# Kernel tuning notes

Measured on AMD Instinct MI355X. Metric: run time of the kernel, lower is better.

Reference implementation:

```python
import jax, jax.numpy as jnp
import numpy as np

EPS = 1e-5


def _bn(a, gamma, beta):
    # training-mode BatchNorm1d applied independently at each timestep:
    # statistics over the batch axis (axis=1) of a [T, B, H] tensor (biased var).
    mu = a.mean(axis=1, keepdims=True)
    var = a.var(axis=1, keepdims=True)
    return gamma * (a - mu) * jax.lax.rsqrt(var + EPS) + beta


def _layer(x, W_xz, b_xz, g_z, beta_z, W_hz, b_hz, W_xh, b_xh, g_h, beta_h, W_hh, b_hh):
    # Precompute the input-side projections + BN for all timesteps (one big GEMM),
    # then scan only the recurrent part.
    az = _bn(jnp.einsum('tbi,hi->tbh', x, W_xz) + b_xz, g_z, beta_z)  # [T,B,H]
    ah = _bn(jnp.einsum('tbi,hi->tbh', x, W_xh) + b_xh, g_h, beta_h)  # [T,B,H]
    B = x.shape[1]
    H = W_hz.shape[0]

    def step(h, inp):
        az_t, ah_t = inp
        Z = jax.nn.sigmoid(az_t + h @ W_hz.T + b_hz)
        Ht = jax.nn.relu(ah_t + h @ W_hh.T + b_hh)
        h2 = Z * h + (1.0 - Z) * Ht
        return h2, h2

    h0 = jnp.zeros((B, H), x.dtype)
    _, ys = jax.lax.scan(step, h0, (az, ah))
    return ys  # [T,B,H]


def setup_inputs() -> dict:
    key = jax.random.key(0)
    T, B, I, H = 500, 64, 512, 1024
    ks = iter(jax.random.split(key, 24))

    def rn(shape, fan):
        return jax.random.normal(next(ks), shape, jnp.float32) / np.sqrt(fan)

    d = {"x": jax.random.normal(next(ks), (T, B, I), jnp.float32)}
    for l, fin in enumerate([I, H]):
        d[f"W_xz{l}"] = rn((H, fin), fin)
        d[f"b_xz{l}"] = rn((H,), fin)
        d[f"g_z{l}"] = jnp.ones((H,), jnp.float32)
        d[f"beta_z{l}"] = jnp.zeros((H,), jnp.float32)
        d[f"W_hz{l}"] = rn((H, H), H)
        d[f"b_hz{l}"] = rn((H,), H)
        d[f"W_xh{l}"] = rn((H, fin), fin)
        d[f"b_xh{l}"] = rn((H,), fin)
        d[f"g_h{l}"] = jnp.ones((H,), jnp.float32)
        d[f"beta_h{l}"] = jnp.zeros((H,), jnp.float32)
        d[f"W_hh{l}"] = rn((H, H), H)
        d[f"b_hh{l}"] = rn((H,), H)
    return d


def reference(x,
              W_xz0, b_xz0, g_z0, beta_z0, W_hz0, b_hz0, W_xh0, b_xh0, g_h0, beta_h0, W_hh0, b_hh0,
              W_xz1, b_xz1, g_z1, beta_z1, W_hz1, b_hz1, W_xh1, b_xh1, g_h1, beta_h1, W_hh1, b_hh1):
    h = _layer(x, W_xz0, b_xz0, g_z0, beta_z0, W_hz0, b_hz0,
               W_xh0, b_xh0, g_h0, beta_h0, W_hh0, b_hh0)
    h = _layer(h, W_xz1, b_xz1, g_z1, beta_z1, W_hz1, b_hz1,
               W_xh1, b_xh1, g_h1, beta_h1, W_hh1, b_hh1)
    return h  # [T, B, hidden_size]
```

## Files before the change

### kernel.cpp

```cpp
#include <hip/hip_runtime.h>

#define TT 500
#define NB_BATCH 64
#define HID 1024
#define NC 2048

typedef __attribute__((ext_vector_type(8))) __bf16 bf16x8;
typedef __attribute__((ext_vector_type(8))) unsigned short us8;
typedef __attribute__((ext_vector_type(4))) unsigned short us4;
typedef __attribute__((ext_vector_type(4))) float f32x4;
typedef __attribute__((ext_vector_type(2))) unsigned long long u64x2;

__device__ __forceinline__ unsigned short f2bf(float f) {
  unsigned u = __builtin_bit_cast(unsigned, f);
  u += 0x7fffu + ((u >> 16) & 1u);
  return (unsigned short)(u >> 16);
}
__device__ __forceinline__ float bf2f(unsigned short h) {
  unsigned u = ((unsigned)h) << 16;
  return __builtin_bit_cast(float, u);
}
__device__ __forceinline__ bf16x8 ld_bf8(const unsigned short* p) {
  return __builtin_bit_cast(bf16x8, *(const us8*)p);
}

#define XS_STR 40
#define WS_STR 40

__global__ __launch_bounds__(256) void proj_bn_kernel(
    const float* __restrict__ X, int K,
    const float* __restrict__ Wxz, const float* __restrict__ Wxh,
    const float* __restrict__ gz, const float* __restrict__ bz,
    const float* __restrict__ gh, const float* __restrict__ bh,
    unsigned short* __restrict__ A)
{
  __shared__ unsigned short Xs[64 * XS_STR];
  __shared__ unsigned short Ws[128 * WS_STR];

  const int t   = blockIdx.x >> 4;
  const int nt  = blockIdx.x & 15;
  const int tid = threadIdx.x;
  const int wave = tid >> 6;
  const int lane = tid & 63;
  const int lm = lane & 15;
  const int lq = lane >> 4;

  const float* Wsrc = (nt < 8) ? (Wxz + (size_t)(nt * 128) * K)
                               : (Wxh + (size_t)((nt - 8) * 128) * K);
  const float* Xbase = X + (size_t)(t * 64) * K;

  f32x4 acc[4][2];
#pragma unroll
  for (int i = 0; i < 4; i++)
#pragma unroll
    for (int j = 0; j < 2; j++) acc[i][j] = (f32x4){0.f, 0.f, 0.f, 0.f};

  const int nkt = K >> 5;
  for (int kt = 0; kt < nkt; ++kt) {
    const int k0 = kt << 5;
#pragma unroll
    for (int it = 0; it < 2; ++it) {
      int idx = it * 256 + tid;
      int r = idx >> 3, c4 = idx & 7;
      float4 v = *(const float4*)(Xbase + (size_t)r * K + k0 + c4 * 4);
      us4 o; o[0] = f2bf(v.x); o[1] = f2bf(v.y); o[2] = f2bf(v.z); o[3] = f2bf(v.w);
      *(us4*)&Xs[r * XS_STR + c4 * 4] = o;
    }
#pragma unroll
    for (int it = 0; it < 4; ++it) {
      int idx = it * 256 + tid;
      int r = idx >> 3, c4 = idx & 7;
      float4 v = *(const float4*)(Wsrc + (size_t)r * K + k0 + c4 * 4);
      us4 o; o[0] = f2bf(v.x); o[1] = f2bf(v.y); o[2] = f2bf(v.z); o[3] = f2bf(v.w);
      *(us4*)&Ws[r * WS_STR + c4 * 4] = o;
    }
    __syncthreads();
    bf16x8 bfr0 = ld_bf8(&Ws[(wave * 32 + lm) * WS_STR + lq * 8]);
    bf16x8 bfr1 = ld_bf8(&Ws[(wave * 32 + 16 + lm) * WS_STR + lq * 8]);
#pragma unroll
    for (int rt = 0; rt < 4; ++rt) {
      bf16x8 afr = ld_bf8(&Xs[(rt * 16 + lm) * XS_STR + lq * 8]);
      acc[rt][0] = __builtin_amdgcn_mfma_f32_16x16x32_bf16(afr, bfr0, acc[rt][0], 0, 0, 0);
      acc[rt][1] = __builtin_amdgcn_mfma_f32_16x16x32_bf16(afr, bfr1, acc[rt][1], 0, 0, 0);
    }
    __syncthreads();
  }

  const float inv64 = 1.0f / 64.0f;
#pragma unroll
  for (int ct = 0; ct < 2; ++ct) {
    float s1 = 0.f, s2 = 0.f;
#pragma unroll
    for (int rt = 0; rt < 4; ++rt)
#pragma unroll
      for (int r = 0; r < 4; ++r) {
        float v = acc[rt][ct][r];
        s1 += v; s2 += v * v;
      }
    s1 += __shfl_xor(s1, 16, 64); s2 += __shfl_xor(s2, 16, 64);
    s1 += __shfl_xor(s1, 32, 64); s2 += __shfl_xor(s2, 32, 64);
    float mean = s1 * inv64;
    float var  = s2 * inv64 - mean * mean;
    int col = nt * 128 + wave * 32 + ct * 16 + lm;
    float g, be;
    if (col < 1024) { g = gz[col];        be = bz[col]; }
    else            { g = gh[col - 1024]; be = bh[col - 1024]; }
    float scale = g * rsqrtf(var + 1e-5f);
    float shift = be - mean * scale;
    unsigned short* Aout = A + (size_t)(t * 64) * NC + col;
#pragma unroll
    for (int rt = 0; rt < 4; ++rt)
#pragma unroll
      for (int r = 0; r < 4; ++r) {
        int b = rt * 16 + lq * 4 + r;
        Aout[(size_t)b * NC] = f2bf(acc[rt][ct][r] * scale + shift);
      }
  }
}

__global__ __launch_bounds__(64) void scan_kernel(
    const unsigned short* __restrict__ A,
    const float* __restrict__ Whz, const float* __restrict__ bhz,
    const float* __restrict__ Whh, const float* __restrict__ bhh,
    unsigned short* __restrict__ hbuf,
    float* __restrict__ ys,
    unsigned* __restrict__ flags)
{
  extern __shared__ unsigned short Wlds[];
  const int lane = threadIdx.x;
  const int fg = blockIdx.x & 63;
  const int bg = blockIdx.x >> 6;
  const int lm = lane & 15;
  const int lq = lane >> 4;
  const int jg = fg * 16 + lm;

  for (int g = 0; g < 2; ++g) {
    const float* Wsrc = (g ? Whh : Whz) + (size_t)(fg * 16) * HID;
#pragma unroll 4
    for (int it = 0; it < 64; ++it) {
      int idx = it * 64 + lane;
      int r = idx >> 8, c4 = idx & 255;
      float4 v = *(const float4*)(Wsrc + (size_t)r * HID + c4 * 4);
      int c = c4 >> 1, hh = c4 & 1;
      us4 o; o[0] = f2bf(v.x); o[1] = f2bf(v.y); o[2] = f2bf(v.z); o[3] = f2bf(v.w);
      *(us4*)&Wlds[g * 16384 + r * 1024 + (((c + 5 * r) & 127) << 3) + hh * 4] = o;
    }
  }
  const float bzv = bhz[jg];
  const float bhv = bhh[jg];
  __syncthreads();

  unsigned short aznx[4], ahnx[4];
  {
    const unsigned short* p = A + (size_t)(bg * 16 + lq * 4) * NC + jg;
#pragma unroll
    for (int r = 0; r < 4; ++r) { aznx[r] = p[(size_t)r * NC]; ahnx[r] = p[(size_t)r * NC + 1024]; }
  }
  float h_own[4] = {0.f, 0.f, 0.f, 0.f};

  unsigned* myflag   = &flags[blockIdx.x * 16];
  unsigned* pollflag = &flags[(bg * 64 + lane) * 16];

  for (int t = 0; t < TT; ++t) {
    f32x4 accz = {0.f, 0.f, 0.f, 0.f}, acch = {0.f, 0.f, 0.f, 0.f};

    unsigned short azc[4], ahc[4];
#pragma unroll
    for (int r = 0; r < 4; ++r) { azc[r] = aznx[r]; ahc[r] = ahnx[r]; }
    if (t + 1 < TT) {
      const unsigned short* p = A + ((size_t)(t + 1) * 64 + bg * 16 + lq * 4) * NC + jg;
#pragma unroll
      for (int r = 0; r < 4; ++r) { aznx[r] = p[(size_t)r * NC]; ahnx[r] = p[(size_t)r * NC + 1024]; }
    }

    if (t > 0) {
      const unsigned tv = (unsigned)t;
      unsigned v = __hip_atomic_load(pollflag, __ATOMIC_RELAXED, __HIP_MEMORY_SCOPE_AGENT);
      while (__ballot(v < tv)) {
        __builtin_amdgcn_s_sleep(1);
        v = __hip_atomic_load(pollflag, __ATOMIC_RELAXED, __HIP_MEMORY_SCOPE_AGENT);
      }
      __atomic_signal_fence(__ATOMIC_SEQ_CST);

      const unsigned long long* hq = (const unsigned long long*)
          (hbuf + (size_t)(t & 1) * 65536 + (size_t)(bg * 16 + lm) * HID) + lq * 2;
      unsigned long long harr[64];
#pragma unroll
      for (int kt = 0; kt < 32; ++kt) {
        harr[2 * kt]     = __hip_atomic_load(hq + kt * 8,     __ATOMIC_RELAXED, __HIP_MEMORY_SCOPE_AGENT);
        harr[2 * kt + 1] = __hip_atomic_load(hq + kt * 8 + 1, __ATOMIC_RELAXED, __HIP_MEMORY_SCOPE_AGENT);
      }
#pragma unroll
      for (int kt = 0; kt < 32; ++kt) {
        u64x2 u; u[0] = harr[2 * kt]; u[1] = harr[2 * kt + 1];
        bf16x8 afr = __builtin_bit_cast(bf16x8, u);
        int c = ((kt * 4 + lq) + 5 * lm) & 127;
        bf16x8 bz8 = ld_bf8(&Wlds[lm * 1024 + c * 8]);
        bf16x8 bh8 = ld_bf8(&Wlds[16384 + lm * 1024 + c * 8]);
        accz = __builtin_amdgcn_mfma_f32_16x16x32_bf16(afr, bz8, accz, 0, 0, 0);
        acch = __builtin_amdgcn_mfma_f32_16x16x32_bf16(afr, bh8, acch, 0, 0, 0);
      }
    }

    unsigned short* hb = hbuf + (size_t)((t + 1) & 1) * 65536;
    unsigned short mybf[4];
#pragma unroll
    for (int r = 0; r < 4; ++r) {
      float z  = 1.0f / (1.0f + __expf(-(bf2f(azc[r]) + accz[r] + bzv)));
      float ht = bf2f(ahc[r]) + acch[r] + bhv;
      ht = ht > 0.f ? ht : 0.f;
      float h2 = z * h_own[r] + (1.0f - z) * ht;
      h_own[r] = h2;
      mybf[r] = f2bf(h2);
    }
#pragma unroll
    for (int r = 0; r < 4; ++r) {
      int p = __shfl((int)mybf[r], lane ^ 1, 64);
      if (!(lane & 1)) {
        unsigned w = (unsigned)mybf[r] | ((unsigned)p << 16);
        int row = bg * 16 + lq * 4 + r;
        __hip_atomic_store((unsigned*)(hb + (size_t)row * HID + jg), w,
                           __ATOMIC_RELAXED, __HIP_MEMORY_SCOPE_AGENT);
      }
    }

    __atomic_signal_fence(__ATOMIC_SEQ_CST);
    __builtin_amdgcn_s_waitcnt(0);
    __atomic_signal_fence(__ATOMIC_SEQ_CST);
    if (lane == 0)
      __hip_atomic_store(myflag, (unsigned)(t + 1), __ATOMIC_RELAXED, __HIP_MEMORY_SCOPE_AGENT);

    float* ysp = ys + ((size_t)t * 64 + bg * 16 + lq * 4) * HID + jg;
#pragma unroll
    for (int r = 0; r < 4; ++r) ysp[(size_t)r * HID] = h_own[r];
  }
}

extern "C" void kernel_launch(void* const* d_in, const int* in_sizes, int n_in,
                              void* d_out, int out_size, void* d_ws, size_t ws_size,
                              hipStream_t stream)
{
  (void)in_sizes; (void)n_in; (void)out_size; (void)ws_size;
  const float* x    = (const float*)d_in[0];
  const float* Wxz0 = (const float*)d_in[1];
  const float* gz0  = (const float*)d_in[3];
  const float* bz0  = (const float*)d_in[4];
  const float* Whz0 = (const float*)d_in[5];
  const float* bhz0 = (const float*)d_in[6];
  const float* Wxh0 = (const float*)d_in[7];
  const float* gh0  = (const float*)d_in[9];
  const float* bh0  = (const float*)d_in[10];
  const float* Whh0 = (const float*)d_in[11];
  const float* bhh0 = (const float*)d_in[12];
  const float* Wxz1 = (const float*)d_in[13];
  const float* gz1  = (const float*)d_in[15];
  const float* bz1  = (const float*)d_in[16];
  const float* Whz1 = (const float*)d_in[17];
  const float* bhz1 = (const float*)d_in[18];
  const float* Wxh1 = (const float*)d_in[19];
  const float* gh1  = (const float*)d_in[21];
  const float* bh1  = (const float*)d_in[22];
  const float* Whh1 = (const float*)d_in[23];
  const float* bhh1 = (const float*)d_in[24];

  char* ws = (char*)d_ws;
  unsigned* flags0 = (unsigned*)(ws);
  unsigned* flags1 = (unsigned*)(ws + 32768);
  unsigned short* hbuf = (unsigned short*)(ws + 65536);
  unsigned short* A    = (unsigned short*)(ws + (1 << 19));
  float* ys0 = (float*)(ws + (1 << 19) + (size_t)TT * 64 * NC * 2);
  float* out = (float*)d_out;

  hipMemsetAsync(ws, 0, 65536, stream);

  proj_bn_kernel<<<dim3(8000), dim3(256), 0, stream>>>(
      x, 512, Wxz0, Wxh0, gz0, bz0, gh0, bh0, A);
  {
    const unsigned short* a0 = A;
    const float* whz = Whz0; const float* vbz = bhz0;
    const float* whh = Whh0; const float* vbh = bhh0;
    unsigned short* hb = hbuf; float* yy = ys0; unsigned* ff = flags0;
    void* kargs[8] = {&a0, &whz, &vbz, &whh, &vbh, &hb, &yy, &ff};
    hipLaunchCooperativeKernel((const void*)scan_kernel, dim3(256), dim3(64),
                               kargs, 65536, stream);
  }
  proj_bn_kernel<<<dim3(8000), dim3(256), 0, stream>>>(
      ys0, 1024, Wxz1, Wxh1, gz1, bz1, gh1, bh1, A);
  {
    const unsigned short* a0 = A;
    const float* whz = Whz1; const float* vbz = bhz1;
    const float* whh = Whh1; const float* vbh = bhh1;
    unsigned short* hb = hbuf; float* yy = out; unsigned* ff = flags1;
    void* kargs[8] = {&a0, &whz, &vbz, &whh, &vbh, &hb, &yy, &ff};
    hipLaunchCooperativeKernel((const void*)scan_kernel, dim3(256), dim3(64),
                               kargs, 65536, stream);
  }
}
```

Measured before the change: 5.225 ms.

## Pre-convert GEMM operands to bf16 and write layer-0 outputs as bf16

Adds a separate fp32-to-bf16 conversion kernel for x and the input projection weights, so the projection GEMM loads bf16 directly and no longer converts inside its inner loop. The layer-0 scan now writes its hidden outputs in bf16 (packed pairs) rather than fp32, which halves that intermediate write and the layer-1 GEMM read. The cost is extra conversion launches and round trips for x and the weights. Layer-1 input precision is unchanged, since it was already rounded to bf16 before.

```diff
diff --git a/kernel.cpp b/kernel.cpp
--- a/kernel.cpp
+++ b/kernel.cpp
@@ -24,12 +24,24 @@
   return __builtin_bit_cast(bf16x8, *(const us8*)p);
 }
 
+__global__ __launch_bounds__(256) void conv_f32_bf16(
+    const float* __restrict__ src, unsigned short* __restrict__ dst)
+{
+  int i = blockIdx.x * 256 + threadIdx.x;
+  const float4* s = (const float4*)src + (size_t)i * 2;
+  float4 a = s[0], b = s[1];
+  us8 o;
+  o[0] = f2bf(a.x); o[1] = f2bf(a.y); o[2] = f2bf(a.z); o[3] = f2bf(a.w);
+  o[4] = f2bf(b.x); o[5] = f2bf(b.y); o[6] = f2bf(b.z); o[7] = f2bf(b.w);
+  *((us8*)dst + i) = o;
+}
+
 #define XS_STR 40
 #define WS_STR 40
 
 __global__ __launch_bounds__(256) void proj_bn_kernel(
-    const float* __restrict__ X, int K,
-    const float* __restrict__ Wxz, const float* __restrict__ Wxh,
+    const unsigned short* __restrict__ X, int K,
+    const unsigned short* __restrict__ Wxz, const unsigned short* __restrict__ Wxh,
     const float* __restrict__ gz, const float* __restrict__ bz,
     const float* __restrict__ gh, const float* __restrict__ bh,
     unsigned short* __restrict__ A)
@@ -45,9 +57,9 @@
   const int lm = lane & 15;
   const int lq = lane >> 4;
 
-  const float* Wsrc = (nt < 8) ? (Wxz + (size_t)(nt * 128) * K)
-                               : (Wxh + (size_t)((nt - 8) * 128) * K);
-  const float* Xbase = X + (size_t)(t * 64) * K;
+  const unsigned short* Wsrc = (nt < 8) ? (Wxz + (size_t)(nt * 128) * K)
+                                        : (Wxh + (size_t)((nt - 8) * 128) * K);
+  const unsigned short* Xbase = X + (size_t)(t * 64) * K;
 
   f32x4 acc[4][2];
 #pragma unroll
@@ -62,17 +74,15 @@
     for (int it = 0; it < 2; ++it) {
       int idx = it * 256 + tid;
       int r = idx >> 3, c4 = idx & 7;
-      float4 v = *(const float4*)(Xbase + (size_t)r * K + k0 + c4 * 4);
-      us4 o; o[0] = f2bf(v.x); o[1] = f2bf(v.y); o[2] = f2bf(v.z); o[3] = f2bf(v.w);
-      *(us4*)&Xs[r * XS_STR + c4 * 4] = o;
+      *(us4*)&Xs[r * XS_STR + c4 * 4] =
+          *(const us4*)(Xbase + (size_t)r * K + k0 + c4 * 4);
     }
 #pragma unroll
     for (int it = 0; it < 4; ++it) {
       int idx = it * 256 + tid;
       int r = idx >> 3, c4 = idx & 7;
-      float4 v = *(const float4*)(Wsrc + (size_t)r * K + k0 + c4 * 4);
-      us4 o; o[0] = f2bf(v.x); o[1] = f2bf(v.y); o[2] = f2bf(v.z); o[3] = f2bf(v.w);
-      *(us4*)&Ws[r * WS_STR + c4 * 4] = o;
+      *(us4*)&Ws[r * WS_STR + c4 * 4] =
+          *(const us4*)(Wsrc + (size_t)r * K + k0 + c4 * 4);
     }
     __syncthreads();
     bf16x8 bfr0 = ld_bf8(&Ws[(wave * 32 + lm) * WS_STR + lq * 8]);
@@ -124,7 +134,8 @@
     const float* __restrict__ Whh, const float* __restrict__ bhh,
     unsigned short* __restrict__ hbuf,
     float* __restrict__ ys,
-    unsigned* __restrict__ flags)
+    unsigned* __restrict__ flags,
+    const int ysfmt)
 {
   extern __shared__ unsigned short Wlds[];
   const int lane = threadIdx.x;
@@ -230,9 +241,22 @@
     if (lane == 0)
       __hip_atomic_store(myflag, (unsigned)(t + 1), __ATOMIC_RELAXED, __HIP_MEMORY_SCOPE_AGENT);
 
-    float* ysp = ys + ((size_t)t * 64 + bg * 16 + lq * 4) * HID + jg;
-#pragma unroll
-    for (int r = 0; r < 4; ++r) ysp[(size_t)r * HID] = h_own[r];
+    if (ysfmt) {
+      float* ysp = ys + ((size_t)t * 64 + bg * 16 + lq * 4) * HID + jg;
+#pragma unroll
+      for (int r = 0; r < 4; ++r) ysp[(size_t)r * HID] = h_own[r];
+    } else {
+      unsigned short* yb = (unsigned short*)ys +
+          ((size_t)t * 64 + bg * 16 + lq * 4) * HID + jg;
+#pragma unroll
+      for (int r = 0; r < 4; ++r) {
+        int p = __shfl((int)mybf[r], lane ^ 1, 64);
+        if (!(lane & 1)) {
+          unsigned w = (unsigned)mybf[r] | ((unsigned)p << 16);
+          *(unsigned*)(yb + (size_t)r * HID) = w;
+        }
+      }
+    }
   }
 }
 
@@ -266,32 +290,45 @@
   char* ws = (char*)d_ws;
   unsigned* flags0 = (unsigned*)(ws);
   unsigned* flags1 = (unsigned*)(ws + 32768);
-  unsigned short* hbuf = (unsigned short*)(ws + 65536);
-  unsigned short* A    = (unsigned short*)(ws + (1 << 19));
-  float* ys0 = (float*)(ws + (1 << 19) + (size_t)TT * 64 * NC * 2);
+  unsigned short* hbuf  = (unsigned short*)(ws + 65536);
+  unsigned short* A     = (unsigned short*)(ws + 524288);
+  unsigned short* ys0bf = (unsigned short*)(ws + 131596288);
+  unsigned short* Xbf   = (unsigned short*)(ws + 197132288);
+  unsigned short* Wzbf  = (unsigned short*)(ws + 229900288);
+  unsigned short* Whbf  = (unsigned short*)(ws + 231997440);
   float* out = (float*)d_out;
 
   hipMemsetAsync(ws, 0, 65536, stream);
 
+  conv_f32_bf16<<<dim3(8000), dim3(256), 0, stream>>>(x, Xbf);
+  conv_f32_bf16<<<dim3(256),  dim3(256), 0, stream>>>(Wxz0, Wzbf);
+  conv_f32_bf16<<<dim3(256),  dim3(256), 0, stream>>>(Wxh0, Whbf);
+
   proj_bn_kernel<<<dim3(8000), dim3(256), 0, stream>>>(
-      x, 512, Wxz0, Wxh0, gz0, bz0, gh0, bh0, A);
+      Xbf, 512, Wzbf, Whbf, gz0, bz0, gh0, bh0, A);
   {
     const unsigned short* a0 = A;
     const float* whz = Whz0; const float* vbz = bhz0;
     const float* whh = Whh0; const float* vbh = bhh0;
-    unsigned short* hb = hbuf; float* yy = ys0; unsigned* ff = flags0;
-    void* kargs[8] = {&a0, &whz, &vbz, &whh, &vbh, &hb, &yy, &ff};
+    unsigned short* hb = hbuf; float* yy = (float*)ys0bf; unsigned* ff = flags0;
+    int fmt = 0;
+    void* kargs[9] = {&a0, &whz, &vbz, &whh, &vbh, &hb, &yy, &ff, &fmt};
     hipLaunchCooperativeKernel((const void*)scan_kernel, dim3(256), dim3(64),
                                kargs, 65536, stream);
   }
+
+  conv_f32_bf16<<<dim3(512), dim3(256), 0, stream>>>(Wxz1, Wzbf);
+  conv_f32_bf16<<<dim3(512), dim3(256), 0, stream>>>(Wxh1, Whbf);
+
   proj_bn_kernel<<<dim3(8000), dim3(256), 0, stream>>>(
-      ys0, 1024, Wxz1, Wxh1, gz1, bz1, gh1, bh1, A);
+      ys0bf, 1024, Wzbf, Whbf, gz1, bz1, gh1, bh1, A);
   {
     const unsigned short* a0 = A;
     const float* whz = Whz1; const float* vbz = bhz1;
     const float* whh = Whh1; const float* vbh = bhh1;
     unsigned short* hb = hbuf; float* yy = out; unsigned* ff = flags1;
-    void* kargs[8] = {&a0, &whz, &vbz, &whh, &vbh, &hb, &yy, &ff};
+    int fmt = 1;
+    void* kargs[9] = {&a0, &whz, &vbz, &whh, &vbh, &hb, &yy, &ff, &fmt};
     hipLaunchCooperativeKernel((const void*)scan_kernel, dim3(256), dim3(64),
                                kargs, 65536, stream);
   }
```

Result: faster. 4.691 ms (-10.2%).
